# Kernel tuning notes

Measured on AMD Instinct MI355X. Metric: run time of the kernel, lower is better.

## Reference

```python
import jax, jax.numpy as jnp
import numpy as np

N_POINTS = 2_000_000
NUM_GRAPHS = 16384
HID = 40  # ffn_param hidden_layer_size
SLOPE = 0.01  # torch default LeakyReLU negative slope


def _w(key, fan_in, fan_out):
    return jax.random.normal(key, (fan_in, fan_out), dtype=jnp.float32) / np.sqrt(fan_in)


def ffn(x, W1, W2, final_linear=False):
    # FFN with n_layers=2, bias=False, hidden=40; dropout is identity in eval.
    h = jax.nn.leaky_relu(x @ W1, SLOPE)
    h = h @ W2
    return h if final_linear else jax.nn.leaky_relu(h, SLOPE)


def setup_inputs() -> dict:
    key = jax.random.key(0)
    ks = jax.random.split(key, 10)
    x = jax.random.normal(ks[0], (N_POINTS, 3), dtype=jnp.float32)
    batch = jnp.sort(jax.random.randint(ks[1], (N_POINTS,), 0, NUM_GRAPHS)).astype(jnp.int64)
    return {
        "x": x,
        "batch": batch,
        # EPiC emb_nn: FFN(3 -> 5)
        "W_emb1": _w(ks[2], 3, HID), "W_emb2": _w(ks[3], HID, 5),
        # EPiC global_nn: FFN(5 -> 4)
        "W_glob1": _w(ks[4], 5, HID), "W_glob2": _w(ks[5], HID, 4),
        # EPiC out_nn: FFN(5+4 -> 32)
        "W_out1": _w(ks[6], 9, HID), "W_out2": _w(ks[7], HID, 32),
        # disc: FFN(32 -> 1, final_linear=True)
        "W_disc1": _w(ks[8], 32, HID), "W_disc2": _w(ks[9], HID, 1),
    }


def reference(x, batch, W_emb1, W_emb2, W_glob1, W_glob2, W_out1, W_out2, W_disc1, W_disc2):
    # EPiC block
    xe = ffn(x, W_emb1, W_emb2)                                   # [N, 5]
    x_aggr = jax.ops.segment_sum(xe, batch, num_segments=NUM_GRAPHS,
                                 indices_are_sorted=True)          # [B, 5]
    x_global = ffn(x_aggr, W_glob1, W_glob2)                       # [B, 4]
    xo = ffn(jnp.concatenate([xe, x_global[batch]], axis=-1),
             W_out1, W_out2)                                       # [N, 32]
    # global pool + final discriminator head
    pooled = jax.ops.segment_sum(xo, batch, num_segments=NUM_GRAPHS,
                                 indices_are_sorted=True)          # [B, 32]
    return ffn(pooled, W_disc1, W_disc2, final_linear=True)        # [B, 1]
```

## Files before the change

kernel.cpp:

```cpp
#include <hip/hip_runtime.h>
#include <hip/hip_bf16.h>

#define N_POINTS   2000000
#define NUM_GRAPHS 16384
#define HID        40
#define SLOPE      0.01f

#define TILE_A     512
#define NT_A       ((N_POINTS + TILE_A - 1) / TILE_A)
#define XESA       584

#define TILE       256
#define NTILES     ((N_POINTS + TILE - 1) / TILE)
#define AROW       20
#define XOS        260

typedef __attribute__((ext_vector_type(8))) short short8;
typedef __attribute__((ext_vector_type(4))) float fx4;

__device__ __forceinline__ float lrelu(float v) { return v > 0.f ? v : SLOPE * v; }
__device__ __forceinline__ int padidx(int p) { return p + ((p >> 5) << 2); }
__device__ __forceinline__ unsigned short f2bf(float f) {
    __hip_bfloat16 h = __float2bfloat16(f);
    return *(unsigned short*)&h;
}
__device__ __forceinline__ float bf2f(unsigned short u) {
    unsigned int v = ((unsigned int)u) << 16;
    return __uint_as_float(v);
}

__global__ __launch_bounds__(256, 2) void k_emb_aggr(
    const float* __restrict__ x, const int* __restrict__ batch,
    const float* __restrict__ We1, const float* __restrict__ We2,
    float* __restrict__ x_aggr, unsigned short* __restrict__ xe_out, int use_xe)
{
    __shared__ __align__(16) float sWe1[3 * HID];
    __shared__ __align__(16) float sWe2T[5 * HID];
    __shared__ __align__(16) float xeT[5 * XESA];
    __shared__ __align__(16) int   sbp[XESA];

    int tid = threadIdx.x;
    for (int k = tid; k < 3 * HID; k += 256) sWe1[k] = We1[k];
    for (int k = tid; k < 5 * HID; k += 256) sWe2T[k] = We2[(k % HID) * 5 + k / HID];
    __syncthreads();

    int base = blockIdx.x * TILE_A;
    int p0 = base + tid, p1 = base + 256 + tid;
    bool v0 = p0 < N_POINTS, v1 = p1 < N_POINTS;
    int i0 = v0 ? p0 : (N_POINTS - 1), i1 = v1 ? p1 : (N_POINTS - 1);
    float a0 = x[i0 * 3 + 0], a1 = x[i0 * 3 + 1], a2 = x[i0 * 3 + 2];
    float c0 = x[i1 * 3 + 0], c1 = x[i1 * 3 + 1], c2 = x[i1 * 3 + 2];
    int b0 = v0 ? batch[i0] : -1;
    int b1 = v1 ? batch[i1] : -1;
    sbp[padidx(tid)] = b0;
    sbp[padidx(256 + tid)] = b1;

    float h0[HID], h1[HID];
    const float4* W1r = (const float4*)sWe1;
#pragma unroll
    for (int j4 = 0; j4 < HID / 4; ++j4) {
        float4 wa = W1r[j4], wb = W1r[10 + j4], wc = W1r[20 + j4];
        float wav[4] = {wa.x, wa.y, wa.z, wa.w};
        float wbv[4] = {wb.x, wb.y, wb.z, wb.w};
        float wcv[4] = {wc.x, wc.y, wc.z, wc.w};
#pragma unroll
        for (int k = 0; k < 4; ++k) {
            int j = j4 * 4 + k;
            h0[j] = lrelu(a0 * wav[k] + a1 * wbv[k] + a2 * wcv[k]);
            h1[j] = lrelu(c0 * wav[k] + c1 * wbv[k] + c2 * wcv[k]);
        }
    }

#pragma unroll
    for (int c = 0; c < 5; ++c) {
        const float4* wr = (const float4*)&sWe2T[c * HID];
        float s0 = 0.f, s1 = 0.f;
#pragma unroll
        for (int j4 = 0; j4 < HID / 4; ++j4) {
            float4 w = wr[j4];
            float wv[4] = {w.x, w.y, w.z, w.w};
#pragma unroll
            for (int k = 0; k < 4; ++k) {
                s0 += h0[j4 * 4 + k] * wv[k];
                s1 += h1[j4 * 4 + k] * wv[k];
            }
        }
        float e0 = v0 ? lrelu(s0) : 0.f;
        float e1 = v1 ? lrelu(s1) : 0.f;
        xeT[c * XESA + padidx(tid)] = e0;
        xeT[c * XESA + padidx(256 + tid)] = e1;
        if (use_xe) {
            if (v0) xe_out[(size_t)c * N_POINTS + p0] = f2bf(e0);
            if (v1) xe_out[(size_t)c * N_POINTS + p1] = f2bf(e1);
        }
    }
    __syncthreads();

    if (tid < 80) {
        int ch = tid >> 4, chunk = tid & 15;
        float acc = 0.f;
        int cur = sbp[chunk * 36];
#pragma unroll
        for (int g = 0; g < 8; ++g) {
            float4 v4 = *(const float4*)&xeT[ch * XESA + chunk * 36 + g * 4];
            int4   n4 = *(const int4*)&sbp[chunk * 36 + g * 4];
            float vv[4] = {v4.x, v4.y, v4.z, v4.w};
            int   nn[4] = {n4.x, n4.y, n4.z, n4.w};
#pragma unroll
            for (int k = 0; k < 4; ++k) {
                if (nn[k] != cur) {
                    if (cur >= 0) atomicAdd(&x_aggr[cur * 5 + ch], acc);
                    cur = nn[k];
                    acc = vv[k];
                } else {
                    acc += vv[k];
                }
            }
        }
        if (cur >= 0) atomicAdd(&x_aggr[cur * 5 + ch], acc);
    }
}

__global__ __launch_bounds__(256) void k_global(
    const float* __restrict__ x_aggr,
    const float* __restrict__ Wg1, const float* __restrict__ Wg2,
    const float* __restrict__ Wo1,
    float* __restrict__ g_contrib)
{
    __shared__ float sWg1[5 * HID];
    __shared__ float sWg2[HID * 4];
    __shared__ float sWo1g[4 * HID];
    for (int k = threadIdx.x; k < 5 * HID; k += 256) sWg1[k] = Wg1[k];
    for (int k = threadIdx.x; k < HID * 4; k += 256) sWg2[k] = Wg2[k];
    for (int k = threadIdx.x; k < 4 * HID; k += 256) sWo1g[k] = Wo1[5 * HID + k];
    __syncthreads();

    int bg = blockIdx.x * 256 + threadIdx.x;
    if (bg >= NUM_GRAPHS) return;

    float a[5];
#pragma unroll
    for (int c = 0; c < 5; ++c) a[c] = x_aggr[bg * 5 + c];

    float h[HID];
#pragma unroll
    for (int j = 0; j < HID; ++j) {
        float s = 0.f;
#pragma unroll
        for (int c = 0; c < 5; ++c) s += a[c] * sWg1[c * HID + j];
        h[j] = lrelu(s);
    }
    float g[4];
#pragma unroll
    for (int c = 0; c < 4; ++c) {
        float s = 0.f;
#pragma unroll
        for (int j = 0; j < HID; ++j) s += h[j] * sWg2[j * 4 + c];
        g[c] = lrelu(s);
    }
#pragma unroll
    for (int j = 0; j < HID; ++j) {
        float s = 0.f;
#pragma unroll
        for (int c = 0; c < 4; ++c) s += g[c] * sWo1g[c * HID + j];
        g_contrib[bg * HID + j] = s;
    }
}

__global__ __launch_bounds__(256, 4) void k_out_pool(
    const float* __restrict__ x, const int* __restrict__ batch,
    const float* __restrict__ We1, const float* __restrict__ We2,
    const float* __restrict__ Wo1, const float* __restrict__ Wo2,
    const float* __restrict__ g_contrib,
    const unsigned short* __restrict__ xe_in, int use_xe,
    float* __restrict__ pooled)
{
    __shared__ __align__(16) unsigned int uLds[32 * XOS];
    __shared__ __align__(16) int sb[TILE];
    __shared__ float sWe1[3 * HID];
    __shared__ float sWe2T[5 * HID];
    __shared__ float sWo1[5 * HID];

    int tid = threadIdx.x;
    for (int k = tid; k < 3 * HID; k += 256) sWe1[k] = We1[k];
    for (int k = tid; k < 5 * HID; k += 256) sWe2T[k] = We2[(k % HID) * 5 + k / HID];
    for (int k = tid; k < 5 * HID; k += 256) sWo1[k] = Wo1[k];

    int lane = tid & 63;
    int l16 = lane & 15, quad = lane >> 4;

    short8 bfrag[2][2];
#pragma unroll
    for (int nt = 0; nt < 2; ++nt) {
#pragma unroll
        for (int ks = 0; ks < 2; ++ks) {
#pragma unroll
            for (int j = 0; j < 8; ++j) {
                int kk = ks * 32 + quad * 8 + j;
                float w = (kk < HID) ? Wo2[kk * 32 + nt * 16 + l16] : 0.f;
                bfrag[nt][ks][j] = (short)f2bf(w);
            }
        }
    }
    short8 zfrag = {0, 0, 0, 0, 0, 0, 0, 0};
    __syncthreads();

    for (int t = blockIdx.x; t < NTILES; t += gridDim.x) {
        int i = t * TILE + tid;
        bool v = i < N_POINTS;
        int ic = v ? i : (N_POINTS - 1);
        int b = v ? batch[ic] : -1;
        sb[tid] = b;

        float xe[5];
        if (use_xe) {
#pragma unroll
            for (int c = 0; c < 5; ++c) xe[c] = bf2f(xe_in[(size_t)c * N_POINTS + ic]);
        } else {
            float x0 = x[ic * 3 + 0], x1 = x[ic * 3 + 1], x2 = x[ic * 3 + 2];
            float h[HID];
            const float4* W1r = (const float4*)sWe1;
#pragma unroll
            for (int j4 = 0; j4 < HID / 4; ++j4) {
                float4 wa = W1r[j4], wb = W1r[10 + j4], wc = W1r[20 + j4];
                float wav[4] = {wa.x, wa.y, wa.z, wa.w};
                float wbv[4] = {wb.x, wb.y, wb.z, wb.w};
                float wcv[4] = {wc.x, wc.y, wc.z, wc.w};
#pragma unroll
                for (int k = 0; k < 4; ++k)
                    h[j4 * 4 + k] = lrelu(x0 * wav[k] + x1 * wbv[k] + x2 * wcv[k]);
            }
#pragma unroll
            for (int c = 0; c < 5; ++c) {
                const float4* wr = (const float4*)&sWe2T[c * HID];
                float s = 0.f;
#pragma unroll
                for (int j4 = 0; j4 < HID / 4; ++j4) {
                    float4 w = wr[j4];
                    s += h[j4 * 4 + 0] * w.x + h[j4 * 4 + 1] * w.y + h[j4 * 4 + 2] * w.z + h[j4 * 4 + 3] * w.w;
                }
                xe[c] = lrelu(s);
            }
        }

        const float4* gc4 = (const float4*)(g_contrib + (size_t)(v ? b : 0) * HID);
        unsigned int* row = &uLds[tid * AROW];
#pragma unroll
        for (int j4 = 0; j4 < HID / 4; ++j4) {
            float4 g = gc4[j4];
            float sv[4] = {g.x, g.y, g.z, g.w};
#pragma unroll
            for (int c = 0; c < 5; ++c) {
                float4 w = ((const float4*)&sWo1[c * HID])[j4];
                float wvv[4] = {w.x, w.y, w.z, w.w};
#pragma unroll
                for (int k = 0; k < 4; ++k) sv[k] += xe[c] * wvv[k];
            }
            __hip_bfloat162 q0 = __float22bfloat162_rn(make_float2(lrelu(sv[0]), lrelu(sv[1])));
            __hip_bfloat162 q1 = __float22bfloat162_rn(make_float2(lrelu(sv[2]), lrelu(sv[3])));
            uint2 u;
            u.x = *(unsigned int*)&q0; u.y = *(unsigned int*)&q1;
            *(uint2*)(row + j4 * 2) = u;
        }

        fx4 xov[4][2];
#pragma unroll
        for (int m = 0; m < 4; ++m) {
            int mt = (tid >> 6) * 4 + m;
            const unsigned int* arow = &uLds[(mt * 16 + l16) * AROW];
            short8 a0 = *(const short8*)(arow + quad * 4);
            short8 a1 = (quad == 0) ? *(const short8*)(arow + 16) : zfrag;
#pragma unroll
            for (int nt = 0; nt < 2; ++nt) {
                fx4 acc = {0.f, 0.f, 0.f, 0.f};
                acc = __builtin_amdgcn_mfma_f32_16x16x32_bf16(a0, bfrag[nt][0], acc, 0, 0, 0);
                acc = __builtin_amdgcn_mfma_f32_16x16x32_bf16(a1, bfrag[nt][1], acc, 0, 0, 0);
#pragma unroll
                for (int r = 0; r < 4; ++r) acc[r] = lrelu(acc[r]);
                xov[m][nt] = acc;
            }
        }
        __syncthreads();

        float* xoT = (float*)uLds;
#pragma unroll
        for (int m = 0; m < 4; ++m) {
            int mt = (tid >> 6) * 4 + m;
#pragma unroll
            for (int nt = 0; nt < 2; ++nt) {
                int ch = nt * 16 + l16;
                int pt = mt * 16 + quad * 4;
                *(fx4*)&xoT[ch * XOS + pt] = xov[m][nt];
            }
        }
        __syncthreads();

        {
            int ch = tid & 31, chunk = tid >> 5;
            float acc = 0.f;
            int cur = sb[chunk * 32];
#pragma unroll
            for (int g = 0; g < 8; ++g) {
                float4 v4 = *(const float4*)&xoT[ch * XOS + chunk * 32 + g * 4];
                int4   n4 = *(const int4*)&sb[chunk * 32 + g * 4];
                float vv[4] = {v4.x, v4.y, v4.z, v4.w};
                int   nn[4] = {n4.x, n4.y, n4.z, n4.w};
#pragma unroll
                for (int k = 0; k < 4; ++k) {
                    if (nn[k] != cur) {
                        if (cur >= 0) atomicAdd(&pooled[cur * 32 + ch], acc);
                        cur = nn[k];
                        acc = vv[k];
                    } else {
                        acc += vv[k];
                    }
                }
            }
            if (cur >= 0) atomicAdd(&pooled[cur * 32 + ch], acc);
        }
        __syncthreads();
    }
}

__global__ __launch_bounds__(256) void k_disc(
    const float* __restrict__ pooled,
    const float* __restrict__ Wd1, const float* __restrict__ Wd2,
    float* __restrict__ out)
{
    __shared__ float sWd1T[HID * 32];
    __shared__ float sWd2[HID];
    for (int k = threadIdx.x; k < 32 * HID; k += 256) sWd1T[k] = Wd1[(k % 32) * HID + k / 32];
    for (int k = threadIdx.x; k < HID; k += 256) sWd2[k] = Wd2[k];
    __syncthreads();

    int bg = blockIdx.x * 256 + threadIdx.x;
    if (bg >= NUM_GRAPHS) return;

    float p[32];
    const float4* pp = (const float4*)(pooled + (size_t)bg * 32);
#pragma unroll
    for (int c4 = 0; c4 < 8; ++c4) {
        float4 vv = pp[c4];
        p[c4 * 4 + 0] = vv.x; p[c4 * 4 + 1] = vv.y; p[c4 * 4 + 2] = vv.z; p[c4 * 4 + 3] = vv.w;
    }

    float acc = 0.f;
#pragma unroll
    for (int j = 0; j < HID; ++j) {
        const float4* wr = (const float4*)&sWd1T[j * 32];
        float s = 0.f;
#pragma unroll
        for (int c4 = 0; c4 < 8; ++c4) {
            float4 w = wr[c4];
            s += p[c4 * 4 + 0] * w.x + p[c4 * 4 + 1] * w.y + p[c4 * 4 + 2] * w.z + p[c4 * 4 + 3] * w.w;
        }
        acc += lrelu(s) * sWd2[j];
    }
    out[bg] = acc;
}

extern "C" void kernel_launch(void* const* d_in, const int* in_sizes, int n_in,
                              void* d_out, int out_size, void* d_ws, size_t ws_size,
                              hipStream_t stream) {
    const float* x     = (const float*)d_in[0];
    const int*   batch = (const int*)  d_in[1];
    const float* We1   = (const float*)d_in[2];
    const float* We2   = (const float*)d_in[3];
    const float* Wg1   = (const float*)d_in[4];
    const float* Wg2   = (const float*)d_in[5];
    const float* Wo1   = (const float*)d_in[6];
    const float* Wo2   = (const float*)d_in[7];
    const float* Wd1   = (const float*)d_in[8];
    const float* Wd2   = (const float*)d_in[9];
    float* out = (float*)d_out;

    float* x_aggr    = (float*)d_ws;
    float* pooled    = x_aggr + NUM_GRAPHS * 5;
    float* g_contrib = pooled + NUM_GRAPHS * 32;
    size_t head_bytes = (size_t)NUM_GRAPHS * (5 + 32 + HID) * sizeof(float);
    unsigned short* xe_ws = (unsigned short*)((char*)d_ws + head_bytes);
    size_t need = head_bytes + (size_t)N_POINTS * 5 * sizeof(unsigned short);
    int use_xe = (ws_size >= need) ? 1 : 0;

    hipMemsetAsync(d_ws, 0, (size_t)NUM_GRAPHS * (5 + 32) * sizeof(float), stream);

    int gblk = (NUM_GRAPHS + 255) / 256;
    k_emb_aggr<<<NT_A, 256, 0, stream>>>(x, batch, We1, We2, x_aggr, xe_ws, use_xe);
    k_global <<<gblk, 256, 0, stream>>>(x_aggr, Wg1, Wg2, Wo1, g_contrib);
    k_out_pool<<<1024, 256, 0, stream>>>(x, batch, We1, We2, Wo1, Wo2, g_contrib,
                                         xe_ws, use_xe, pooled);
    k_disc   <<<gblk, 256, 0, stream>>>(pooled, Wd1, Wd2, out);
}
```

Measured before the change: 192.0 us.

## Pack xe as interleaved bf16x8, prefetch next tile, shrink LDS for more occupancy

The intermediate xe buffer changes from channel-planar bf16 to one 16-byte packed record per point, so both kernels use a single vector store and load instead of five strided scalar accesses. k_out_pool prefetches the next tile's batch ids and xe into registers to overlap global loads with compute. Its LDS shrinks by transposing and pooling the 32 output channels in two halves of 16, and occupancy is raised (launch bounds 6, grid 1536). In exchange the xe buffer grows from 10 to 16 bytes per point, and the halved pooling adds an extra barrier pass per tile.

```diff
diff --git a/kernel.cpp b/kernel.cpp
--- a/kernel.cpp
+++ b/kernel.cpp
@@ -14,6 +14,7 @@
 #define NTILES     ((N_POINTS + TILE - 1) / TILE)
 #define AROW       20
 #define XOS        260
+#define GRID_C     1536
 
 typedef __attribute__((ext_vector_type(8))) short short8;
 typedef __attribute__((ext_vector_type(4))) float fx4;
@@ -24,12 +25,14 @@
     __hip_bfloat16 h = __float2bfloat16(f);
     return *(unsigned short*)&h;
 }
-__device__ __forceinline__ float bf2f(unsigned short u) {
-    unsigned int v = ((unsigned int)u) << 16;
-    return __uint_as_float(v);
-}
-
-__global__ __launch_bounds__(256, 2) void k_emb_aggr(
+__device__ __forceinline__ unsigned int packbf2(float a, float b) {
+    __hip_bfloat162 p = __float22bfloat162_rn(make_float2(a, b));
+    return *(unsigned int*)&p;
+}
+__device__ __forceinline__ float bflo(unsigned int d) { return __uint_as_float(d << 16); }
+__device__ __forceinline__ float bfhi(unsigned int d) { return __uint_as_float(d & 0xffff0000u); }
+
+__global__ __launch_bounds__(256) void k_emb_aggr(
     const float* __restrict__ x, const int* __restrict__ batch,
     const float* __restrict__ We1, const float* __restrict__ We2,
     float* __restrict__ x_aggr, unsigned short* __restrict__ xe_out, int use_xe)
@@ -71,6 +74,7 @@
         }
     }
 
+    float e0v[5], e1v[5];
 #pragma unroll
     for (int c = 0; c < 5; ++c) {
         const float4* wr = (const float4*)&sWe2T[c * HID];
@@ -85,13 +89,23 @@
                 s1 += h1[j4 * 4 + k] * wv[k];
             }
         }
-        float e0 = v0 ? lrelu(s0) : 0.f;
-        float e1 = v1 ? lrelu(s1) : 0.f;
-        xeT[c * XESA + padidx(tid)] = e0;
-        xeT[c * XESA + padidx(256 + tid)] = e1;
-        if (use_xe) {
-            if (v0) xe_out[(size_t)c * N_POINTS + p0] = f2bf(e0);
-            if (v1) xe_out[(size_t)c * N_POINTS + p1] = f2bf(e1);
+        e0v[c] = v0 ? lrelu(s0) : 0.f;
+        e1v[c] = v1 ? lrelu(s1) : 0.f;
+        xeT[c * XESA + padidx(tid)] = e0v[c];
+        xeT[c * XESA + padidx(256 + tid)] = e1v[c];
+    }
+    if (use_xe) {
+        if (v0) {
+            uint4 u;
+            u.x = packbf2(e0v[0], e0v[1]); u.y = packbf2(e0v[2], e0v[3]);
+            u.z = packbf2(e0v[4], 0.f);    u.w = 0u;
+            *(uint4*)&xe_out[(size_t)p0 * 8] = u;
+        }
+        if (v1) {
+            uint4 u;
+            u.x = packbf2(e1v[0], e1v[1]); u.y = packbf2(e1v[2], e1v[3]);
+            u.z = packbf2(e1v[4], 0.f);    u.w = 0u;
+            *(uint4*)&xe_out[(size_t)p1 * 8] = u;
         }
     }
     __syncthreads();
@@ -167,7 +181,7 @@
     }
 }
 
-__global__ __launch_bounds__(256, 4) void k_out_pool(
+__global__ __launch_bounds__(256, 6) void k_out_pool(
     const float* __restrict__ x, const int* __restrict__ batch,
     const float* __restrict__ We1, const float* __restrict__ We2,
     const float* __restrict__ Wo1, const float* __restrict__ Wo2,
@@ -175,7 +189,7 @@
     const unsigned short* __restrict__ xe_in, int use_xe,
     float* __restrict__ pooled)
 {
-    __shared__ __align__(16) unsigned int uLds[32 * XOS];
+    __shared__ __align__(16) unsigned int uLds[TILE * AROW];
     __shared__ __align__(16) int sb[TILE];
     __shared__ float sWe1[3 * HID];
     __shared__ float sWe2T[5 * HID];
@@ -205,17 +219,39 @@
     short8 zfrag = {0, 0, 0, 0, 0, 0, 0, 0};
     __syncthreads();
 
-    for (int t = blockIdx.x; t < NTILES; t += gridDim.x) {
+    int t = blockIdx.x;
+    int pb = -1;
+    uint4 pxe = {0u, 0u, 0u, 0u};
+    {
         int i = t * TILE + tid;
         bool v = i < N_POINTS;
         int ic = v ? i : (N_POINTS - 1);
-        int b = v ? batch[ic] : -1;
+        pb = v ? batch[ic] : -1;
+        if (use_xe) pxe = *(const uint4*)&xe_in[(size_t)ic * 8];
+    }
+
+    for (; t < NTILES; t += GRID_C) {
+        int i = t * TILE + tid;
+        bool v = i < N_POINTS;
+        int ic = v ? i : (N_POINTS - 1);
+        int b = pb;
+        uint4 xe4 = pxe;
         sb[tid] = b;
+
+        int tn = t + GRID_C;
+        if (tn < NTILES) {
+            int i2 = tn * TILE + tid;
+            bool v2 = i2 < N_POINTS;
+            int ic2 = v2 ? i2 : (N_POINTS - 1);
+            pb = v2 ? batch[ic2] : -1;
+            if (use_xe) pxe = *(const uint4*)&xe_in[(size_t)ic2 * 8];
+        }
 
         float xe[5];
         if (use_xe) {
-#pragma unroll
-            for (int c = 0; c < 5; ++c) xe[c] = bf2f(xe_in[(size_t)c * N_POINTS + ic]);
+            xe[0] = bflo(xe4.x); xe[1] = bfhi(xe4.x);
+            xe[2] = bflo(xe4.y); xe[3] = bfhi(xe4.y);
+            xe[4] = bflo(xe4.z);
         } else {
             float x0 = x[ic * 3 + 0], x1 = x[ic * 3 + 1], x2 = x[ic * 3 + 2];
             float h[HID];
@@ -256,10 +292,9 @@
 #pragma unroll
                 for (int k = 0; k < 4; ++k) sv[k] += xe[c] * wvv[k];
             }
-            __hip_bfloat162 q0 = __float22bfloat162_rn(make_float2(lrelu(sv[0]), lrelu(sv[1])));
-            __hip_bfloat162 q1 = __float22bfloat162_rn(make_float2(lrelu(sv[2]), lrelu(sv[3])));
             uint2 u;
-            u.x = *(unsigned int*)&q0; u.y = *(unsigned int*)&q1;
+            u.x = packbf2(lrelu(sv[0]), lrelu(sv[1]));
+            u.y = packbf2(lrelu(sv[2]), lrelu(sv[3]));
             *(uint2*)(row + j4 * 2) = u;
         }
 
@@ -283,42 +318,41 @@
         __syncthreads();
 
         float* xoT = (float*)uLds;
-#pragma unroll
-        for (int m = 0; m < 4; ++m) {
-            int mt = (tid >> 6) * 4 + m;
-#pragma unroll
-            for (int nt = 0; nt < 2; ++nt) {
-                int ch = nt * 16 + l16;
+#pragma unroll 1
+        for (int half = 0; half < 2; ++half) {
+#pragma unroll
+            for (int m = 0; m < 4; ++m) {
+                int mt = (tid >> 6) * 4 + m;
                 int pt = mt * 16 + quad * 4;
-                *(fx4*)&xoT[ch * XOS + pt] = xov[m][nt];
-            }
-        }
-        __syncthreads();
-
-        {
-            int ch = tid & 31, chunk = tid >> 5;
-            float acc = 0.f;
-            int cur = sb[chunk * 32];
-#pragma unroll
-            for (int g = 0; g < 8; ++g) {
-                float4 v4 = *(const float4*)&xoT[ch * XOS + chunk * 32 + g * 4];
-                int4   n4 = *(const int4*)&sb[chunk * 32 + g * 4];
-                float vv[4] = {v4.x, v4.y, v4.z, v4.w};
-                int   nn[4] = {n4.x, n4.y, n4.z, n4.w};
-#pragma unroll
-                for (int k = 0; k < 4; ++k) {
-                    if (nn[k] != cur) {
-                        if (cur >= 0) atomicAdd(&pooled[cur * 32 + ch], acc);
-                        cur = nn[k];
-                        acc = vv[k];
-                    } else {
-                        acc += vv[k];
+                *(fx4*)&xoT[l16 * XOS + pt] = xov[m][half];
+            }
+            __syncthreads();
+
+            if (tid < 128) {
+                int ch = tid & 15, chunk = tid >> 4;
+                float acc = 0.f;
+                int cur = sb[chunk * 32];
+#pragma unroll
+                for (int g = 0; g < 8; ++g) {
+                    float4 v4 = *(const float4*)&xoT[ch * XOS + chunk * 32 + g * 4];
+                    int4   n4 = *(const int4*)&sb[chunk * 32 + g * 4];
+                    float vv[4] = {v4.x, v4.y, v4.z, v4.w};
+                    int   nn[4] = {n4.x, n4.y, n4.z, n4.w};
+#pragma unroll
+                    for (int k = 0; k < 4; ++k) {
+                        if (nn[k] != cur) {
+                            if (cur >= 0) atomicAdd(&pooled[cur * 32 + half * 16 + ch], acc);
+                            cur = nn[k];
+                            acc = vv[k];
+                        } else {
+                            acc += vv[k];
+                        }
                     }
                 }
-            }
-            if (cur >= 0) atomicAdd(&pooled[cur * 32 + ch], acc);
-        }
-        __syncthreads();
+                if (cur >= 0) atomicAdd(&pooled[cur * 32 + half * 16 + ch], acc);
+            }
+            __syncthreads();
+        }
     }
 }
 
@@ -379,7 +413,7 @@
     float* g_contrib = pooled + NUM_GRAPHS * 32;
     size_t head_bytes = (size_t)NUM_GRAPHS * (5 + 32 + HID) * sizeof(float);
     unsigned short* xe_ws = (unsigned short*)((char*)d_ws + head_bytes);
-    size_t need = head_bytes + (size_t)N_POINTS * 5 * sizeof(unsigned short);
+    size_t need = head_bytes + (size_t)N_POINTS * 8 * sizeof(unsigned short);
     int use_xe = (ws_size >= need) ? 1 : 0;
 
     hipMemsetAsync(d_ws, 0, (size_t)NUM_GRAPHS * (5 + 32) * sizeof(float), stream);
@@ -387,7 +421,7 @@
     int gblk = (NUM_GRAPHS + 255) / 256;
     k_emb_aggr<<<NT_A, 256, 0, stream>>>(x, batch, We1, We2, x_aggr, xe_ws, use_xe);
     k_global <<<gblk, 256, 0, stream>>>(x_aggr, Wg1, Wg2, Wo1, g_contrib);
-    k_out_pool<<<1024, 256, 0, stream>>>(x, batch, We1, We2, Wo1, Wo2, g_contrib,
-                                         xe_ws, use_xe, pooled);
+    k_out_pool<<<GRID_C, 256, 0, stream>>>(x, batch, We1, We2, Wo1, Wo2, g_contrib,
+                                           xe_ws, use_xe, pooled);
     k_disc   <<<gblk, 256, 0, stream>>>(pooled, Wd1, Wd2, out);
 }
```

New measurement: 311.0 us. 1.62x slower.
